# Performance work log

Measured on AMD Instinct MI355X. Metric: run time of the kernel, lower is better.

## Reference

```python
import jax, jax.numpy as jnp
import numpy as np

N_EMBD = 512
HEADS = 8
PATCH = 16
STRIDE = 4
NUM_POINTS = 128


def pos_embed_sine(n_embd=N_EMBD, patch=PATCH, temperature=10000.0):
    # getPositionEmbeddingSine(num_pos_feats=n_embd, patch=16, normalize=True)
    ar = np.arange(patch, dtype=np.float32)
    yy, xx = np.meshgrid(ar, ar, indexing='ij')  # torch.meshgrid default 'ij'
    eps, scale = 1e-6, 2.0 * np.pi
    y_e = yy / (yy[-1:, :] + eps) * scale
    x_e = xx / (xx[:, -1:] + eps) * scale
    dim_t = np.arange(n_embd // 2, dtype=np.float32)
    dim_t = temperature ** (2.0 * np.floor(dim_t / 2.0) / n_embd)
    px = x_e[:, :, None] / dim_t
    py = y_e[:, :, None] / dim_t
    px = np.stack((np.sin(px[:, :, 0::2]), np.cos(px[:, :, 1::2])), axis=3).reshape(patch, patch, -1)
    py = np.stack((np.sin(py[:, :, 0::2]), np.cos(py[:, :, 1::2])), axis=3).reshape(patch, patch, -1)
    pos = np.concatenate((py, px), axis=2).transpose(2, 0, 1)  # [n_embd, patch, patch]
    return jnp.asarray(pos, jnp.float32)


def setup_inputs() -> dict:
    key = jax.random.key(0)
    ks = jax.random.split(key, 6)
    B, T, C, H, W = 32, 64, 64, 160, 160
    h = w = 640  # input image size (feature stride 4)
    N = B * T
    cnn_feature = jax.random.normal(ks[0], (B, C, H, W), jnp.float32)
    contours = jax.random.uniform(ks[1], (N, NUM_POINTS, 2), jnp.float32) * w  # image-space coords
    ct_01 = jnp.ones((B, T), bool)
    ct_img_idx = jnp.repeat(jnp.arange(B, dtype=jnp.int32), T)
    ct_ind = jax.random.randint(ks[2], (N,), 0, H * W, jnp.int32)
    conv_w = jax.random.normal(ks[3], (N_EMBD, C + 2, NUM_POINTS // STRIDE), jnp.float32) * 0.02
    conv_b = jnp.zeros((N_EMBD,), jnp.float32)
    attn_w = jax.random.normal(ks[4], (2 * N_EMBD, N_EMBD), jnp.float32) * 0.02
    attn_b = jnp.zeros((2 * N_EMBD,), jnp.float32)
    p_w = jax.random.normal(ks[5], (1, HEADS, 1), jnp.float32)
    pos_embed = pos_embed_sine()
    return dict(cnn_feature=cnn_feature, contours=contours, ct_01=ct_01,
                ct_img_idx=ct_img_idx, ct_ind=ct_ind, h=h, w=w,
                conv_w=conv_w, conv_b=conv_b, attn_w=attn_w, attn_b=attn_b,
                p_w=p_w, pos_embed=pos_embed)


def _forward(cnn_feature, contours, ct_01, ct_img_idx, ct_ind, h, w,
             conv_w, conv_b, attn_w, attn_b, p_w, pos_embed):
    B, C, H, W = cnn_feature.shape
    Bp, T = ct_01.shape
    N = contours.shape[0]
    cs = contours[:, ::STRIDE]  # [N, P, 2] sampled contour points
    # grid_sample bilinear, align_corners=False, zeros padding:
    # pixel = ((x/(w/2)-1 + 1)*W - 1)/2 = x*W/w - 0.5
    px = cs[..., 0] * (float(W) / float(w)) - 0.5
    py = cs[..., 1] * (float(H) / float(h)) - 0.5
    x0 = jnp.floor(px)
    y0 = jnp.floor(py)

    def gather(yi, xi, wgt):
        valid = (xi >= 0) & (xi < W) & (yi >= 0) & (yi < H)
        xi_c = jnp.clip(xi, 0, W - 1).astype(jnp.int32)
        yi_c = jnp.clip(yi, 0, H - 1).astype(jnp.int32)
        v = cnn_feature[ct_img_idx[:, None], :, yi_c, xi_c]  # [N, P, C]
        return v * (wgt * valid)[..., None]

    feats = (gather(y0, x0, (x0 + 1 - px) * (y0 + 1 - py))
             + gather(y0, x0 + 1, (px - x0) * (y0 + 1 - py))
             + gather(y0 + 1, x0, (x0 + 1 - px) * (py - y0))
             + gather(y0 + 1, x0 + 1, (px - x0) * (py - y0)))
    feats = feats.transpose(0, 2, 1)  # [N, C, P]
    normed = (cs / jnp.array([w, h], jnp.float32)).transpose(0, 2, 1)  # [N, 2, P]
    cf = jnp.concatenate([feats, normed], axis=1)  # [N, C+2, P]
    # Conv1d with kernel == full length -> a single contraction over (channel, point)
    cf = jnp.einsum('ncp,ocp->no', cf, conv_w) + conv_b  # [N, n_embd]
    # positional embedding indexed by quantized center coords
    ct_x = (ct_ind % W) * PATCH // W
    ct_y = (ct_ind // W) * PATCH // H
    cf = cf + pos_embed[:, ct_y, ct_x].T  # [N, n_embd]
    qk = cf @ attn_w.T + attn_b
    q, k = qk[:, :N_EMBD], qk[:, N_EMBD:]
    # boolean-mask scatter into padded [B, T, E] (row-major fill order)
    mask = ct_01.reshape(-1)
    order = jnp.clip(jnp.cumsum(mask) - 1, 0, N - 1)
    pad_q = jnp.where(mask[:, None], q[order], 0.0).reshape(Bp, T, N_EMBD)
    pad_k = jnp.where(mask[:, None], k[order], 0.0).reshape(Bp, T, N_EMBD)
    hd = N_EMBD // HEADS
    Q = pad_q.reshape(Bp, T, HEADS, hd).transpose(0, 2, 1, 3)
    K = pad_k.reshape(Bp, T, HEADS, hd).transpose(0, 2, 1, 3)
    att = jnp.einsum('bhtd,bhsd->bhts', Q, K) * (1.0 / jnp.sqrt(jnp.float32(hd)))
    # registered 'bias' buffer is all ones -> masked_fill is a no-op
    att = jnp.einsum('bhts,h->bts', att, p_w[0, :, 0])  # 1x1 conv across heads
    att = jax.nn.sigmoid(att)
    return jnp.where(jnp.isnan(att), 0.0, att)


def reference(cnn_feature, contours, ct_01, ct_img_idx, ct_ind, h, w,
              conv_w, conv_b, attn_w, attn_b, p_w, pos_embed):
    return _forward(cnn_feature, contours, ct_01, ct_img_idx, ct_ind, h, w,
                    conv_w, conv_b, attn_w, attn_b, p_w, pos_embed)
```

## Files before the change

kernel.cpp:

```cpp
#include <hip/hip_runtime.h>
#include <math.h>

#define NCT   2048
#define BIMG  32
#define CIN   64
#define CTOT  66
#define NPTS  32
#define KCONV 2112
#define NE    512
#define NQK   1024
#define HH    160
#define WW    160
#define NROWS (BIMG * HH)
#define CAP   128

typedef __attribute__((ext_vector_type(8))) short short8;
typedef __attribute__((ext_vector_type(4))) float f32x4;

#define OFF_WT    0
#define OFF_AWT   (OFF_WT + 540672)
#define OFF_XA    (OFF_AWT + 262144)
#define OFF_XB    (OFF_XA + 2162688)
#define OFF_CF    (OFF_XB + 2162688)
#define OFF_PART  (OFF_CF + 524288)
#define OFF_QKB   (OFF_PART + 4194304)
#define OFF_PTS   (OFF_QKB + 1048576)
#define OFF_CNT   (OFF_PTS + 131072)
#define OFF_LIST  (OFF_CNT + 5120)

__device__ __forceinline__ unsigned short f2bf(float f) {
    unsigned int u = __float_as_uint(f);
    u += 0x7FFFu + ((u >> 16) & 1u);
    return (unsigned short)(u >> 16);
}
__device__ __forceinline__ float bf2f(unsigned int h) {
    return __uint_as_float(h << 16);
}
__device__ __forceinline__ unsigned int bfadd2(unsigned int a, unsigned int b) {
    float lo = bf2f(a & 0xFFFFu) + bf2f(b & 0xFFFFu);
    float hi = __uint_as_float(a & 0xFFFF0000u) + __uint_as_float(b & 0xFFFF0000u);
    return (unsigned int)f2bf(lo) | ((unsigned int)f2bf(hi) << 16);
}
__device__ __forceinline__ uint4 bfadd8(uint4 a, uint4 b) {
    return make_uint4(bfadd2(a.x, b.x), bfadd2(a.y, b.y),
                      bfadd2(a.z, b.z), bfadd2(a.w, b.w));
}

__global__ void __launch_bounds__(256)
k_pre(const float* __restrict__ conv_w, const float* __restrict__ attn_w,
      const float* __restrict__ contours, const int* __restrict__ img_idx,
      unsigned short* __restrict__ Wt, unsigned short* __restrict__ Awt,
      float* __restrict__ pts, int* __restrict__ cnt, int* __restrict__ list,
      unsigned short* __restrict__ Xa, unsigned short* __restrict__ Xb) {
    int bid = blockIdx.x;
    if (bid < 512) {
        const float* src = conv_w + (size_t)bid * KCONV;
        unsigned short* dst = Wt + (size_t)bid * KCONV;
        for (int k2 = threadIdx.x; k2 < KCONV; k2 += 256) {
            int p = k2 / CTOT;
            int c = k2 - p * CTOT;
            dst[k2] = f2bf(src[c * NPTS + p]);
        }
    } else if (bid < 1024) {
        int i = ((bid - 512) * 256 + threadIdx.x) * 4;
        float4 v = *(const float4*)(attn_w + i);
        uint2 o;
        o.x = (unsigned int)f2bf(v.x) | ((unsigned int)f2bf(v.y) << 16);
        o.y = (unsigned int)f2bf(v.z) | ((unsigned int)f2bf(v.w) << 16);
        *(uint2*)(Awt + i) = o;
    } else {
        __shared__ int lcnt[HH];
        int ig = bid - 1024;
        int img = img_idx[ig * 64];
        for (int j = threadIdx.x; j < HH; j += 256) lcnt[j] = 0;
        __syncthreads();
        for (int k = threadIdx.x; k < 64 * NPTS; k += 256) {
            int n = ig * 64 + (k >> 5), p = k & 31;
            int pid = n * NPTS + p;
            float cx = contours[(n * 128 + p * 4) * 2 + 0];
            float cy = contours[(n * 128 + p * 4) * 2 + 1];
            float px = cx * 0.25f - 0.5f;
            float py = cy * 0.25f - 0.5f;
            pts[pid * 2 + 0] = px;
            pts[pid * 2 + 1] = py;
            int y0 = (int)floorf(py);
#pragma unroll
            for (int r = 0; r < 2; ++r) {
                int yc = min(max(y0 + r, 0), HH - 1);
                int slot = atomicAdd(&lcnt[yc], 1);
                if (slot < CAP) list[(img * HH + yc) * CAP + slot] = pid | (r << 16);
            }
            size_t base = (size_t)n * KCONV + p * CTOT;
            Xa[base + 64] = f2bf(cx * (1.f / 640.f));
            Xa[base + 65] = f2bf(cy * (1.f / 640.f));
            Xb[base + 64] = 0;
            Xb[base + 65] = 0;
        }
        __syncthreads();
        for (int j = threadIdx.x; j < HH; j += 256) cnt[img * HH + j] = lcnt[j];
    }
}

__global__ void __launch_bounds__(256)
k_stage(const float* __restrict__ feat, const float* __restrict__ pts,
        const int* __restrict__ cnt, const int* __restrict__ list,
        unsigned short* __restrict__ Xa, unsigned short* __restrict__ Xb) {
    __shared__ float sA[32 * 161];
    int bid = blockIdx.x;
    int chalf = bid & 1;
    int rowid = bid >> 1;
    int img = rowid / HH, row = rowid % HH;
    int nE = min(cnt[rowid], CAP);
    if (nE == 0) return;

    const float* fbase = feat + ((size_t)img * CIN + chalf * 32) * (HH * WW) + row * WW;
#pragma unroll
    for (int i = 0; i < 5; ++i) {
        int idx = threadIdx.x + i * 256;
        int c = idx / 40, xq = idx % 40;
        float4 v = *(const float4*)(fbase + (size_t)c * (HH * WW) + xq * 4);
        float* s = &sA[c * 161 + xq * 4];
        s[0] = v.x; s[1] = v.y; s[2] = v.z; s[3] = v.w;
    }
    __syncthreads();

    int sub = threadIdx.x >> 5;
    int ch = threadIdx.x & 31;
    for (int e = sub; e < nE; e += 8) {
        int entry = list[rowid * CAP + e];
        int pid = entry & 0xFFFF, r = entry >> 16;
        float px = pts[pid * 2 + 0];
        float py = pts[pid * 2 + 1];
        float fx0 = floorf(px), fy0 = floorf(py);
        int x0 = (int)fx0;
        float wx1 = px - fx0, wx0 = 1.f - wx1;
        float wy = r ? (py - fy0) : (fy0 + 1.f - py);
        int yi = (int)fy0 + r;
        bool vy = (yi >= 0) & (yi < HH);
        bool vx0 = (x0 >= 0) & (x0 < WW);
        bool vx1 = (x0 + 1 >= 0) & (x0 + 1 < WW);
        int xc0 = min(max(x0, 0), WW - 1);
        int xc1 = min(max(x0 + 1, 0), WW - 1);
        float v0 = sA[ch * 161 + xc0];
        float v1 = sA[ch * 161 + xc1];
        float contrib = vy ? wy * ((vx0 ? wx0 * v0 : 0.f) + (vx1 ? wx1 * v1 : 0.f))
                           : 0.f;
        int n = pid >> 5, p = pid & 31;
        unsigned short* dst = r ? Xb : Xa;
        dst[(size_t)n * KCONV + p * CTOT + chalf * 32 + ch] = f2bf(contrib);
    }
}

template <bool SUM2>
__device__ __forceinline__ void mm64core(const unsigned short* __restrict__ A,
                                         const unsigned short* __restrict__ A2, int lda,
                                         const unsigned short* __restrict__ B, int ldb,
                                         int m0, int n0, int kbeg, int ksteps,
                                         f32x4 acc[2][2]) {
    __shared__ unsigned short As[64 * 40];
    __shared__ unsigned short Bs[64 * 40];
    const int t = threadIdx.x;
    const int ra = t >> 2;
    const int ca = (t & 3) << 3;
    const int wid = t >> 6, lane = t & 63;
    const int wm = (wid >> 1) << 5, wn = (wid & 1) << 5;
    const int fr = lane & 15, kg = lane >> 4;

    const unsigned short* pa = A + (size_t)(m0 + ra) * lda + kbeg + ca;
    const unsigned short* pa2 = SUM2 ? (A2 + (size_t)(m0 + ra) * lda + kbeg + ca) : nullptr;
    const unsigned short* pb = B + (size_t)(n0 + ra) * ldb + kbeg + ca;
    uint4 va = *(const uint4*)pa;
    uint4 va2 = SUM2 ? *(const uint4*)pa2 : make_uint4(0, 0, 0, 0);
    uint4 vb = *(const uint4*)pb;

    for (int s = 0; s < ksteps; ++s) {
        uint4 sa = SUM2 ? bfadd8(va, va2) : va;
        __syncthreads();
        *(uint4*)&As[ra * 40 + ca] = sa;
        *(uint4*)&Bs[ra * 40 + ca] = vb;
        __syncthreads();
        if (s + 1 < ksteps) {
            va = *(const uint4*)(pa + (s + 1) * 32);
            if (SUM2) va2 = *(const uint4*)(pa2 + (s + 1) * 32);
            vb = *(const uint4*)(pb + (s + 1) * 32);
        }
        short8 a0 = *(const short8*)&As[(wm + fr) * 40 + kg * 8];
        short8 a1 = *(const short8*)&As[(wm + 16 + fr) * 40 + kg * 8];
        short8 b0 = *(const short8*)&Bs[(wn + fr) * 40 + kg * 8];
        short8 b1 = *(const short8*)&Bs[(wn + 16 + fr) * 40 + kg * 8];
        acc[0][0] = __builtin_amdgcn_mfma_f32_16x16x32_bf16(a0, b0, acc[0][0], 0, 0, 0);
        acc[0][1] = __builtin_amdgcn_mfma_f32_16x16x32_bf16(a0, b1, acc[0][1], 0, 0, 0);
        acc[1][0] = __builtin_amdgcn_mfma_f32_16x16x32_bf16(a1, b0, acc[1][0], 0, 0, 0);
        acc[1][1] = __builtin_amdgcn_mfma_f32_16x16x32_bf16(a1, b1, acc[1][1], 0, 0, 0);
    }
}

__global__ void __launch_bounds__(256)
k_mm_conv(const unsigned short* __restrict__ Xa, const unsigned short* __restrict__ Xb,
          const unsigned short* __restrict__ Wt, float* __restrict__ part) {
    f32x4 acc[2][2] = {};
    int m0 = blockIdx.x * 64, n0 = blockIdx.y * 64, kz = blockIdx.z;
    int kbeg = (kz < 2) ? kz * 544 : 1088 + (kz - 2) * 512;
    int ksteps = (kz < 2) ? 17 : 16;
    mm64core<true>(Xa, Xb, KCONV, Wt, KCONV, m0, n0, kbeg, ksteps, acc);
    int lane = threadIdx.x & 63, wid = threadIdx.x >> 6;
    int wm = (wid >> 1) << 5, wn = (wid & 1) << 5;
    int crow = (lane >> 4) * 4, ccol = lane & 15;
    float* dst = part + (size_t)kz * (NCT * NE);
#pragma unroll
    for (int i = 0; i < 2; ++i)
#pragma unroll
        for (int j = 0; j < 2; ++j)
#pragma unroll
            for (int r = 0; r < 4; ++r)
                dst[(size_t)(m0 + wm + i * 16 + crow + r) * NE + (n0 + wn + j * 16 + ccol)] = acc[i][j][r];
}

__global__ void k_cf(const float* __restrict__ part, const float* __restrict__ conv_b,
                     const float* __restrict__ pos, const int* __restrict__ ct_ind,
                     unsigned short* __restrict__ cf) {
    int idx = blockIdx.x * blockDim.x + threadIdx.x;
    int n = idx >> 7, og = (idx & 127) << 2;
    int ct = ct_ind[n];
    int ctx = ((ct % WW) * 16) / WW;
    int cty = ((ct / WW) * 16) / HH;
    float s[4] = {0.f, 0.f, 0.f, 0.f};
#pragma unroll
    for (int kz = 0; kz < 4; ++kz) {
        float4 p = *(const float4*)(part + ((size_t)kz * NCT + n) * NE + og);
        s[0] += p.x; s[1] += p.y; s[2] += p.z; s[3] += p.w;
    }
    float4 cb = *(const float4*)(conv_b + og);
    s[0] += cb.x + pos[((og + 0) * 16 + cty) * 16 + ctx];
    s[1] += cb.y + pos[((og + 1) * 16 + cty) * 16 + ctx];
    s[2] += cb.z + pos[((og + 2) * 16 + cty) * 16 + ctx];
    s[3] += cb.w + pos[((og + 3) * 16 + cty) * 16 + ctx];
    uint2 o;
    o.x = (unsigned int)f2bf(s[0]) | ((unsigned int)f2bf(s[1]) << 16);
    o.y = (unsigned int)f2bf(s[2]) | ((unsigned int)f2bf(s[3]) << 16);
    *(uint2*)(cf + (size_t)n * NE + og) = o;
}

__global__ void __launch_bounds__(256)
k_mm_attn(const unsigned short* __restrict__ cf, const unsigned short* __restrict__ Awt,
          const float* __restrict__ attn_b, const float* __restrict__ pw,
          unsigned short* __restrict__ qkb) {
    f32x4 acc[2][2] = {};
    int m0 = blockIdx.x * 64, n0 = blockIdx.y * 64;
    mm64core<false>(cf, nullptr, NE, Awt, NE, m0, n0, 0, 16, acc);
    int lane = threadIdx.x & 63, wid = threadIdx.x >> 6;
    int wm = (wid >> 1) << 5, wn = (wid & 1) << 5;
    int crow = (lane >> 4) * 4, ccol = lane & 15;
#pragma unroll
    for (int i = 0; i < 2; ++i)
#pragma unroll
        for (int j = 0; j < 2; ++j) {
            int o = n0 + wn + j * 16 + ccol;
            float scale = (o < NE) ? pw[o >> 6] * 0.125f : 1.f;
            float bias = attn_b[o];
#pragma unroll
            for (int r = 0; r < 4; ++r) {
                float v = (acc[i][j][r] + bias) * scale;
                qkb[(size_t)(m0 + wm + i * 16 + crow + r) * NQK + o] = f2bf(v);
            }
        }
}

__global__ void __launch_bounds__(256)
k_att2(const unsigned short* __restrict__ qkb, float* __restrict__ out) {
    f32x4 acc[2][2] = {};
    int b = blockIdx.x;
    const unsigned short* base = qkb + (size_t)b * 64 * NQK;
    mm64core<false>(base, nullptr, NQK, base + NE, NQK, 0, 0, 0, 16, acc);
    int lane = threadIdx.x & 63, wid = threadIdx.x >> 6;
    int wm = (wid >> 1) << 5, wn = (wid & 1) << 5;
    int crow = (lane >> 4) * 4, ccol = lane & 15;
    float* dst = out + (size_t)b * 4096;
#pragma unroll
    for (int i = 0; i < 2; ++i)
#pragma unroll
        for (int j = 0; j < 2; ++j)
#pragma unroll
            for (int r = 0; r < 4; ++r) {
                float s = acc[i][j][r];
                float sg = 1.f / (1.f + expf(-s));
                sg = (sg == sg) ? sg : 0.f;
                dst[(wm + i * 16 + crow + r) * 64 + (wn + j * 16 + ccol)] = sg;
            }
}

extern "C" void kernel_launch(void* const* d_in, const int* in_sizes, int n_in,
                              void* d_out, int out_size, void* d_ws, size_t ws_size,
                              hipStream_t stream) {
    const float* cnn      = (const float*)d_in[0];
    const float* contours = (const float*)d_in[1];
    const int* img_idx    = (const int*)d_in[3];
    const int* ct_ind     = (const int*)d_in[4];
    const float* conv_w   = (const float*)d_in[7];
    const float* conv_b   = (const float*)d_in[8];
    const float* attn_w   = (const float*)d_in[9];
    const float* attn_b   = (const float*)d_in[10];
    const float* p_w      = (const float*)d_in[11];
    const float* pos      = (const float*)d_in[12];

    float* ws = (float*)d_ws;
    unsigned short* Wt  = (unsigned short*)(ws + OFF_WT);
    unsigned short* Awt = (unsigned short*)(ws + OFF_AWT);
    unsigned short* Xa  = (unsigned short*)(ws + OFF_XA);
    unsigned short* Xb  = (unsigned short*)(ws + OFF_XB);
    unsigned short* cf  = (unsigned short*)(ws + OFF_CF);
    float* part = ws + OFF_PART;
    unsigned short* qkb = (unsigned short*)(ws + OFF_QKB);
    float* pts  = ws + OFF_PTS;
    int*   cnt  = (int*)(ws + OFF_CNT);
    int*   list = (int*)(ws + OFF_LIST);
    float* out  = (float*)d_out;

    hipLaunchKernelGGL(k_pre,     dim3(1056),      dim3(256), 0, stream,
                       conv_w, attn_w, contours, img_idx, Wt, Awt, pts, cnt, list, Xa, Xb);
    hipLaunchKernelGGL(k_stage,   dim3(2 * NROWS), dim3(256), 0, stream, cnn, pts, cnt, list, Xa, Xb);
    hipLaunchKernelGGL(k_mm_conv, dim3(32, 8, 4),  dim3(256), 0, stream, Xa, Xb, Wt, part);
    hipLaunchKernelGGL(k_cf,      dim3(1024),      dim3(256), 0, stream, part, conv_b, pos, ct_ind, cf);
    hipLaunchKernelGGL(k_mm_attn, dim3(32, 16),    dim3(256), 0, stream, cf, Awt, attn_b, p_w, qkb);
    hipLaunchKernelGGL(k_att2,    dim3(32),        dim3(256), 0, stream, qkb, out);
}
```

Measured before the change: 101.6 us.

## Fuse split-K reduction and attention epilogue via last-block atomic tickets

Removes the separate k_cf and k_att2 launches. The last block to finish each output tile now does that work inside the preceding GEMM, using an atomic ticket counter per tile that is zeroed by an extra block in k_pre. This cuts two kernel launches and their inter-kernel gaps. In exchange, the tail work is serialized on whichever block finishes last, and correctness now relies on threadfence ordering and on the counters being reset every call.

```diff
diff --git a/kernel.cpp b/kernel.cpp
--- a/kernel.cpp
+++ b/kernel.cpp
@@ -27,6 +27,7 @@
 #define OFF_PTS   (OFF_QKB + 1048576)
 #define OFF_CNT   (OFF_PTS + 131072)
 #define OFF_LIST  (OFF_CNT + 5120)
+#define OFF_TICK  (OFF_LIST + 655360)
 
 __device__ __forceinline__ unsigned short f2bf(float f) {
     unsigned int u = __float_as_uint(f);
@@ -51,7 +52,8 @@
       const float* __restrict__ contours, const int* __restrict__ img_idx,
       unsigned short* __restrict__ Wt, unsigned short* __restrict__ Awt,
       float* __restrict__ pts, int* __restrict__ cnt, int* __restrict__ list,
-      unsigned short* __restrict__ Xa, unsigned short* __restrict__ Xb) {
+      unsigned short* __restrict__ Xa, unsigned short* __restrict__ Xb,
+      int* __restrict__ tick) {
     int bid = blockIdx.x;
     if (bid < 512) {
         const float* src = conv_w + (size_t)bid * KCONV;
@@ -68,7 +70,7 @@
         o.x = (unsigned int)f2bf(v.x) | ((unsigned int)f2bf(v.y) << 16);
         o.y = (unsigned int)f2bf(v.z) | ((unsigned int)f2bf(v.w) << 16);
         *(uint2*)(Awt + i) = o;
-    } else {
+    } else if (bid < 1056) {
         __shared__ int lcnt[HH];
         int ig = bid - 1024;
         int img = img_idx[ig * 64];
@@ -98,6 +100,8 @@
         }
         __syncthreads();
         for (int j = threadIdx.x; j < HH; j += 256) cnt[img * HH + j] = lcnt[j];
+    } else {
+        for (int j = threadIdx.x; j < 288; j += 256) tick[j] = 0;
     }
 }
 
@@ -197,9 +201,13 @@
 
 __global__ void __launch_bounds__(256)
 k_mm_conv(const unsigned short* __restrict__ Xa, const unsigned short* __restrict__ Xb,
-          const unsigned short* __restrict__ Wt, float* __restrict__ part) {
+          const unsigned short* __restrict__ Wt, float* __restrict__ part,
+          const float* __restrict__ conv_b, const float* __restrict__ pos,
+          const int* __restrict__ ct_ind, unsigned short* __restrict__ cf,
+          int* __restrict__ tick) {
     f32x4 acc[2][2] = {};
-    int m0 = blockIdx.x * 64, n0 = blockIdx.y * 64, kz = blockIdx.z;
+    int bm = blockIdx.x, bn = blockIdx.y, kz = blockIdx.z;
+    int m0 = bm * 64, n0 = bn * 64;
     int kbeg = (kz < 2) ? kz * 544 : 1088 + (kz - 2) * 512;
     int ksteps = (kz < 2) ? 17 : 16;
     mm64core<true>(Xa, Xb, KCONV, Wt, KCONV, m0, n0, kbeg, ksteps, acc);
@@ -214,39 +222,47 @@
 #pragma unroll
             for (int r = 0; r < 4; ++r)
                 dst[(size_t)(m0 + wm + i * 16 + crow + r) * NE + (n0 + wn + j * 16 + ccol)] = acc[i][j][r];
-}
-
-__global__ void k_cf(const float* __restrict__ part, const float* __restrict__ conv_b,
-                     const float* __restrict__ pos, const int* __restrict__ ct_ind,
-                     unsigned short* __restrict__ cf) {
-    int idx = blockIdx.x * blockDim.x + threadIdx.x;
-    int n = idx >> 7, og = (idx & 127) << 2;
-    int ct = ct_ind[n];
-    int ctx = ((ct % WW) * 16) / WW;
-    int cty = ((ct / WW) * 16) / HH;
-    float s[4] = {0.f, 0.f, 0.f, 0.f};
-#pragma unroll
-    for (int kz = 0; kz < 4; ++kz) {
-        float4 p = *(const float4*)(part + ((size_t)kz * NCT + n) * NE + og);
-        s[0] += p.x; s[1] += p.y; s[2] += p.z; s[3] += p.w;
-    }
-    float4 cb = *(const float4*)(conv_b + og);
-    s[0] += cb.x + pos[((og + 0) * 16 + cty) * 16 + ctx];
-    s[1] += cb.y + pos[((og + 1) * 16 + cty) * 16 + ctx];
-    s[2] += cb.z + pos[((og + 2) * 16 + cty) * 16 + ctx];
-    s[3] += cb.w + pos[((og + 3) * 16 + cty) * 16 + ctx];
-    uint2 o;
-    o.x = (unsigned int)f2bf(s[0]) | ((unsigned int)f2bf(s[1]) << 16);
-    o.y = (unsigned int)f2bf(s[2]) | ((unsigned int)f2bf(s[3]) << 16);
-    *(uint2*)(cf + (size_t)n * NE + og) = o;
+
+    __shared__ int isLast;
+    __syncthreads();
+    __threadfence();
+    if (threadIdx.x == 0)
+        isLast = (atomicAdd(&tick[bm * 8 + bn], 1) == 3);
+    __syncthreads();
+    if (!isLast) return;
+    __threadfence();
+    for (int e = threadIdx.x; e < 1024; e += 256) {
+        int row = e >> 4, og = (e & 15) << 2;
+        int n = m0 + row, o = n0 + og;
+        float s0 = 0.f, s1 = 0.f, s2 = 0.f, s3 = 0.f;
+#pragma unroll
+        for (int k4 = 0; k4 < 4; ++k4) {
+            float4 p = *(const float4*)(part + ((size_t)k4 * NCT + n) * NE + o);
+            s0 += p.x; s1 += p.y; s2 += p.z; s3 += p.w;
+        }
+        int ct = ct_ind[n];
+        int ctx = ((ct % WW) * 16) / WW;
+        int cty = ((ct / WW) * 16) / HH;
+        float4 cb = *(const float4*)(conv_b + o);
+        s0 += cb.x + pos[((o + 0) * 16 + cty) * 16 + ctx];
+        s1 += cb.y + pos[((o + 1) * 16 + cty) * 16 + ctx];
+        s2 += cb.z + pos[((o + 2) * 16 + cty) * 16 + ctx];
+        s3 += cb.w + pos[((o + 3) * 16 + cty) * 16 + ctx];
+        uint2 ov;
+        ov.x = (unsigned int)f2bf(s0) | ((unsigned int)f2bf(s1) << 16);
+        ov.y = (unsigned int)f2bf(s2) | ((unsigned int)f2bf(s3) << 16);
+        *(uint2*)(cf + (size_t)n * NE + o) = ov;
+    }
 }
 
 __global__ void __launch_bounds__(256)
 k_mm_attn(const unsigned short* __restrict__ cf, const unsigned short* __restrict__ Awt,
           const float* __restrict__ attn_b, const float* __restrict__ pw,
-          unsigned short* __restrict__ qkb) {
+          unsigned short* __restrict__ qkb, float* __restrict__ out,
+          int* __restrict__ tick2) {
     f32x4 acc[2][2] = {};
-    int m0 = blockIdx.x * 64, n0 = blockIdx.y * 64;
+    int bm = blockIdx.x;
+    int m0 = bm * 64, n0 = blockIdx.y * 64;
     mm64core<false>(cf, nullptr, NE, Awt, NE, m0, n0, 0, 16, acc);
     int lane = threadIdx.x & 63, wid = threadIdx.x >> 6;
     int wm = (wid >> 1) << 5, wn = (wid & 1) << 5;
@@ -264,25 +280,26 @@
                 qkb[(size_t)(m0 + wm + i * 16 + crow + r) * NQK + o] = f2bf(v);
             }
         }
-}
-
-__global__ void __launch_bounds__(256)
-k_att2(const unsigned short* __restrict__ qkb, float* __restrict__ out) {
-    f32x4 acc[2][2] = {};
-    int b = blockIdx.x;
-    const unsigned short* base = qkb + (size_t)b * 64 * NQK;
-    mm64core<false>(base, nullptr, NQK, base + NE, NQK, 0, 0, 0, 16, acc);
-    int lane = threadIdx.x & 63, wid = threadIdx.x >> 6;
-    int wm = (wid >> 1) << 5, wn = (wid & 1) << 5;
-    int crow = (lane >> 4) * 4, ccol = lane & 15;
-    float* dst = out + (size_t)b * 4096;
+
+    __shared__ int isLast;
+    __syncthreads();
+    __threadfence();
+    if (threadIdx.x == 0)
+        isLast = (atomicAdd(&tick2[bm], 1) == 15);
+    __syncthreads();
+    if (!isLast) return;
+    __threadfence();
+    f32x4 acc2[2][2] = {};
+    const unsigned short* base = qkb + (size_t)bm * 64 * NQK;
+    mm64core<false>(base, nullptr, NQK, base + NE, NQK, 0, 0, 0, 16, acc2);
+    float* dst = out + (size_t)bm * 4096;
 #pragma unroll
     for (int i = 0; i < 2; ++i)
 #pragma unroll
         for (int j = 0; j < 2; ++j)
 #pragma unroll
             for (int r = 0; r < 4; ++r) {
-                float s = acc[i][j][r];
+                float s = acc2[i][j][r];
                 float sg = 1.f / (1.f + expf(-s));
                 sg = (sg == sg) ? sg : 0.f;
                 dst[(wm + i * 16 + crow + r) * 64 + (wn + j * 16 + ccol)] = sg;
@@ -314,13 +331,14 @@
     float* pts  = ws + OFF_PTS;
     int*   cnt  = (int*)(ws + OFF_CNT);
     int*   list = (int*)(ws + OFF_LIST);
+    int*   tick = (int*)(ws + OFF_TICK);
     float* out  = (float*)d_out;
 
-    hipLaunchKernelGGL(k_pre,     dim3(1056),      dim3(256), 0, stream,
-                       conv_w, attn_w, contours, img_idx, Wt, Awt, pts, cnt, list, Xa, Xb);
+    hipLaunchKernelGGL(k_pre,     dim3(1057),      dim3(256), 0, stream,
+                       conv_w, attn_w, contours, img_idx, Wt, Awt, pts, cnt, list, Xa, Xb, tick);
     hipLaunchKernelGGL(k_stage,   dim3(2 * NROWS), dim3(256), 0, stream, cnn, pts, cnt, list, Xa, Xb);
-    hipLaunchKernelGGL(k_mm_conv, dim3(32, 8, 4),  dim3(256), 0, stream, Xa, Xb, Wt, part);
-    hipLaunchKernelGGL(k_cf,      dim3(1024),      dim3(256), 0, stream, part, conv_b, pos, ct_ind, cf);
-    hipLaunchKernelGGL(k_mm_attn, dim3(32, 16),    dim3(256), 0, stream, cf, Awt, attn_b, p_w, qkb);
-    hipLaunchKernelGGL(k_att2,    dim3(32),        dim3(256), 0, stream, qkb, out);
-}
+    hipLaunchKernelGGL(k_mm_conv, dim3(32, 8, 4),  dim3(256), 0, stream,
+                       Xa, Xb, Wt, part, conv_b, pos, ct_ind, cf, tick);
+    hipLaunchKernelGGL(k_mm_attn, dim3(32, 16),    dim3(256), 0, stream,
+                       cf, Awt, attn_b, p_w, qkb, out, tick + 256);
+}
```

Measured after the change: 288.3 us. 184% more time.
